# Kernel tuning notes

Hardware: AMD Instinct MI355X
Metric: run time of the kernel (lower is better)

## Reference

```python
import math
import jax, jax.numpy as jnp
import numpy as np

B, T, D, HS = 8, 2048, 1024, 64  # batch, seq (== block_size), d_embed, head_size
BLOCK_SIZE = 2048


def setup_inputs() -> dict:
    key = jax.random.key(0)
    kx, kq, kk, kv = jax.random.split(key, 4)
    x = jax.random.normal(kx, (B, T, D), dtype=jnp.float32)
    Wq = jax.random.normal(kq, (D, HS), dtype=jnp.float32) * (1.0 / math.sqrt(D))
    Wk = jax.random.normal(kk, (D, HS), dtype=jnp.float32) * (1.0 / math.sqrt(D))
    Wv = jax.random.normal(kv, (D, HS), dtype=jnp.float32) * (1.0 / math.sqrt(D))
    return {"x": x, "Wq": Wq, "Wk": Wk, "Wv": Wv}


def reference(x, Wq, Wk, Wv):
    # q, k, v: [B, T, HS]
    q = jnp.einsum("btd,dh->bth", x, Wq)
    k = jnp.einsum("btd,dh->bth", x, Wk)
    v = jnp.einsum("btd,dh->bth", x, Wv)
    # NOTE: original scales by 1/sqrt(block_size), not 1/sqrt(head_size)
    scale = 1.0 / math.sqrt(BLOCK_SIZE)
    scores = jnp.einsum("bqh,bkh->bqk", q, k) * scale  # [B, T, T]
    Tq = x.shape[1]
    causal = jnp.tril(jnp.ones((Tq, Tq), dtype=bool))
    scores = jnp.where(causal[None, :, :], scores, -jnp.inf)
    attn = jax.nn.softmax(scores, axis=-1)
    return jnp.einsum("bqk,bkh->bqh", attn, v)  # [B, T, HS]
```

## Files before the change

### kernel.cpp

```cpp
#include <hip/hip_runtime.h>

typedef unsigned short u16;
typedef unsigned int u32;
typedef float f32x4 __attribute__((ext_vector_type(4)));
typedef short s16x8 __attribute__((ext_vector_type(8)));

#define MFMA_BF16(a, b, c) __builtin_amdgcn_mfma_f32_16x16x32_bf16((a), (b), (c), 0, 0, 0)


__device__ __forceinline__ u16 f2bf(float f) {
  union { float f; u32 u; } v; v.f = f;
  u32 u = v.u;
  return (u16)((u + 0x7FFFu + ((u >> 16) & 1u)) >> 16);
}

__global__ __launch_bounds__(256) void wt_convert(const float* __restrict__ Wq,
                                                  const float* __restrict__ Wk,
                                                  const float* __restrict__ Wv,
                                                  u16* __restrict__ Wt) {
  int idx = blockIdx.x * 256 + threadIdx.x;
  if (idx >= 192 * 1024) return;
  int row = idx >> 10, d = idx & 1023;
  int m = row >> 6, h = row & 63;
  const float* W = (m == 0) ? Wq : (m == 1) ? Wk : Wv;
  Wt[idx] = f2bf(W[d * 64 + h]);
}

__global__ __launch_bounds__(512) void qkv_gemm(const float* __restrict__ x,
                                                const u16* __restrict__ Wt,
                                                u16* __restrict__ qo,
                                                u16* __restrict__ ko,
                                                u16* __restrict__ vTo) {
  __shared__ u16 Xs[2][32][88];
  __shared__ u16 Ws[2][192][88];
  const int tid = threadIdx.x;
  const int lane = tid & 63, w = tid >> 6;
  const int lc = lane & 15, hi = lane >> 4;
  const int m0 = blockIdx.x * 32;
  const int msub = w >> 2;
  const int nbase = (w & 3) * 3;

  f32x4 acc[3];
#pragma unroll
  for (int i = 0; i < 3; ++i) acc[i] = (f32x4){0.f, 0.f, 0.f, 0.f};

  const int xrow = tid >> 4, xcol = (tid & 15) * 4;
  const int wr0r = tid >> 3, wr0c = (tid & 7) * 8;
  const int wr1r = (tid + 512) >> 3, wr1c = ((tid + 512) & 7) * 8;
  const int wr2r = (tid + 1024) >> 3, wr2c = ((tid + 1024) & 7) * 8;

  float4 xr;
  uint4 wv0, wv1, wv2;
  auto issue_loads = [&](int k0) {
    xr = *(const float4*)(x + (size_t)(m0 + xrow) * 1024 + k0 + xcol);
    wv0 = *(const uint4*)&Wt[wr0r * 1024 + k0 + wr0c];
    wv1 = *(const uint4*)&Wt[wr1r * 1024 + k0 + wr1c];
    wv2 = *(const uint4*)&Wt[wr2r * 1024 + k0 + wr2c];
  };
  auto write_stage = [&](int bf) {
    u32 plo = (u32)f2bf(xr.x) | ((u32)f2bf(xr.y) << 16);
    u32 phi = (u32)f2bf(xr.z) | ((u32)f2bf(xr.w) << 16);
    *(uint2*)&Xs[bf][xrow][xcol] = make_uint2(plo, phi);
    *(uint4*)&Ws[bf][wr0r][wr0c] = wv0;
    *(uint4*)&Ws[bf][wr1r][wr1c] = wv1;
    *(uint4*)&Ws[bf][wr2r][wr2c] = wv2;
  };

  issue_loads(0);
  write_stage(0);
  __syncthreads();
  int cur = 0;

  for (int t = 0; t < 16; ++t) {
    if (t < 15) issue_loads((t + 1) * 64);
#pragma unroll
    for (int ksub = 0; ksub < 2; ++ksub) {
      s16x8 a = *(const s16x8*)&Xs[cur][msub * 16 + lc][ksub * 32 + hi * 8];
#pragma unroll
      for (int j = 0; j < 3; ++j) {
        s16x8 bfrag = *(const s16x8*)&Ws[cur][(nbase + j) * 16 + lc][ksub * 32 + hi * 8];
        acc[j] = MFMA_BF16(a, bfrag, acc[j]);
      }
    }
    if (t < 15) {
      write_stage(cur ^ 1);
      __syncthreads();
      cur ^= 1;
    }
  }

#pragma unroll
  for (int j = 0; j < 3; ++j) {
    int nt = nbase + j;
#pragma unroll
    for (int r = 0; r < 4; ++r) {
      int gr = m0 + msub * 16 + hi * 4 + r;
      u16 val = f2bf(acc[j][r]);
      int n = nt * 16 + lc;
      if (nt < 4) {
        qo[gr * 64 + n] = val;
      } else if (nt < 8) {
        ko[gr * 64 + (n - 64)] = val;
      } else {
        int b = gr >> 11, t2 = gr & 2047;
        vTo[((b << 6) + (n - 128)) * 2048 + t2] = val;
      }
    }
  }
}

__global__ __launch_bounds__(1024) void attn_fwd(const u16* __restrict__ qb,
                                                 const u16* __restrict__ kb,
                                                 const u16* __restrict__ vT,
                                                 float* __restrict__ out) {
  __shared__ u16 P[16][16][40];
  __shared__ float Po[16][16][66];
  __shared__ float Pl[16][16];
  const int tid = threadIdx.x, lane = tid & 63, w = tid >> 6;
  const int lc = lane & 15, hi = lane >> 4;
  const int q = w >> 2, s = w & 3;
  const int bid = blockIdx.x;
  const int b = bid & 7, pr = bid >> 3;
  const int tile = (q < 2) ? pr : 63 - pr;
  const int qbase = tile * 32 + (q & 1) * 16;
  const int brow = b * 2048;

  const u16* qrow = qb + (size_t)(brow + qbase + lc) * 64;
  s16x8 aq0 = *(const s16x8*)(qrow + hi * 8);
  s16x8 aq1 = *(const s16x8*)(qrow + 32 + hi * 8);

  f32x4 o[4];
  float lrow[4] = {0.f, 0.f, 0.f, 0.f};
#pragma unroll
  for (int i = 0; i < 4; ++i) o[i] = (f32x4){0.f, 0.f, 0.f, 0.f};

  const float SL = 0.031879357f;
  const int n = (qbase + 47) >> 5;
  const int c = (n + 3) >> 2;
  const int it0 = s * c;
  const int it1 = min(it0 + c, n);

  const u16* kbase = kb + (size_t)brow * 64;
  s16x8 k00, k01, k10, k11;
  if (it0 < it1) {
    const u16* krow = kbase + (size_t)(it0 * 32) * 64;
    k00 = *(const s16x8*)(krow + lc * 64 + hi * 8);
    k01 = *(const s16x8*)(krow + lc * 64 + 32 + hi * 8);
    k10 = *(const s16x8*)(krow + (16 + lc) * 64 + hi * 8);
    k11 = *(const s16x8*)(krow + (16 + lc) * 64 + 32 + hi * 8);
  }

  for (int it = it0; it < it1; ++it) {
    const int kvb = it * 32;
    s16x8 n00, n01, n10, n11;
    if (it + 1 < it1) {
      const u16* krow = kbase + (size_t)(kvb + 32) * 64;
      n00 = *(const s16x8*)(krow + lc * 64 + hi * 8);
      n01 = *(const s16x8*)(krow + lc * 64 + 32 + hi * 8);
      n10 = *(const s16x8*)(krow + (16 + lc) * 64 + hi * 8);
      n11 = *(const s16x8*)(krow + (16 + lc) * 64 + 32 + hi * 8);
    }
    f32x4 s0 = {0.f, 0.f, 0.f, 0.f}, s1 = {0.f, 0.f, 0.f, 0.f};
    s0 = MFMA_BF16(aq0, k00, s0);
    s0 = MFMA_BF16(aq1, k01, s0);
    s1 = MFMA_BF16(aq0, k10, s1);
    s1 = MFMA_BF16(aq1, k11, s1);

    s16x8 bv[4];
#pragma unroll
    for (int nt = 0; nt < 4; ++nt)
      bv[nt] = *(const s16x8*)&vT[(size_t)(b * 64 + nt * 16 + lc) * 2048 + kvb + hi * 8];

#pragma unroll
    for (int r = 0; r < 4; ++r) {
      const int qt = qbase + hi * 4 + r;
      const int kv0 = kvb + lc;
      float p0 = (kv0 <= qt) ? exp2f(s0[r] * SL) : 0.f;
      float p1 = (kv0 + 16 <= qt) ? exp2f(s1[r] * SL) : 0.f;
      lrow[r] += p0 + p1;
      P[w][hi * 4 + r][lc] = f2bf(p0);
      P[w][hi * 4 + r][16 + lc] = f2bf(p1);
    }
    asm volatile("s_waitcnt lgkmcnt(0)" ::: "memory");
    s16x8 pa = *(const s16x8*)&P[w][lc][hi * 8];
#pragma unroll
    for (int nt = 0; nt < 4; ++nt) o[nt] = MFMA_BF16(pa, bv[nt], o[nt]);

    if (it + 1 < it1) { k00 = n00; k01 = n01; k10 = n10; k11 = n11; }
  }

#pragma unroll
  for (int r = 0; r < 4; ++r) {
    lrow[r] += __shfl_xor(lrow[r], 1);
    lrow[r] += __shfl_xor(lrow[r], 2);
    lrow[r] += __shfl_xor(lrow[r], 4);
    lrow[r] += __shfl_xor(lrow[r], 8);
  }

  if (lc == 0) {
#pragma unroll
    for (int r = 0; r < 4; ++r) Pl[w][hi * 4 + r] = lrow[r];
  }
#pragma unroll
  for (int nt = 0; nt < 4; ++nt) {
#pragma unroll
    for (int r = 0; r < 4; ++r) Po[w][hi * 4 + r][nt * 16 + lc] = o[nt][r];
  }
  __syncthreads();

  if (s == 0) {
#pragma unroll 4
    for (int row = 0; row < 16; ++row) {
      float L = Pl[w][row] + Pl[w + 1][row] + Pl[w + 2][row] + Pl[w + 3][row];
      float val = Po[w][row][lane] + Po[w + 1][row][lane] +
                  Po[w + 2][row][lane] + Po[w + 3][row][lane];
      out[(size_t)(brow + qbase + row) * 64 + lane] = val / L;
    }
  }
}

extern "C" void kernel_launch(void* const* d_in, const int* in_sizes, int n_in,
                              void* d_out, int out_size, void* d_ws, size_t ws_size,
                              hipStream_t stream) {
  (void)in_sizes; (void)n_in; (void)out_size; (void)ws_size;
  const float* x = (const float*)d_in[0];
  const float* Wq = (const float*)d_in[1];
  const float* Wk = (const float*)d_in[2];
  const float* Wv = (const float*)d_in[3];
  float* out = (float*)d_out;

  u16* wsu = (u16*)d_ws;
  u16* Wt = wsu;
  u16* qb = Wt + 192 * 1024;
  u16* kb = qb + 8 * 2048 * 64;
  u16* vT = kb + 8 * 2048 * 64;

  wt_convert<<<768, 256, 0, stream>>>(Wq, Wk, Wv, Wt);
  qkv_gemm<<<512, 512, 0, stream>>>(x, Wt, qb, kb, vT);
  attn_fwd<<<256, 1024, 0, stream>>>(qb, kb, vT, out);
}
```

Measured before the change: 62.59 us.

## Rework weight transpose, load GEMM weights to registers, split attention across more waves

The weight convert kernel now transposes through shared memory in 64x64 tiles with coalesced vector reads and writes, using far fewer blocks. The QKV GEMM drops the shared-memory weight stage and loads B fragments straight from global into registers with double buffering. Attention switches to 16-row query tiles, each split across 8 key-range waves (512 blocks), adds a mask-free fast path for fully visible blocks, and uses truncating bf16 conversion for P. The combine step reuses one unioned shared buffer. Risks are more register pressure, extra cross-wave reduction work, and slightly lower P precision from truncation.

Result: slower. 132.8 us (+112.1%).

```diff
diff --git a/kernel.cpp b/kernel.cpp
--- a/kernel.cpp
+++ b/kernel.cpp
@@ -13,26 +13,51 @@
   u32 u = v.u;
   return (u16)((u + 0x7FFFu + ((u >> 16) & 1u)) >> 16);
 }
+__device__ __forceinline__ u16 f2bf_t(float f) {
+  union { float f; u32 u; } v; v.f = f;
+  return (u16)(v.u >> 16);
+}
 
 __global__ __launch_bounds__(256) void wt_convert(const float* __restrict__ Wq,
                                                   const float* __restrict__ Wk,
                                                   const float* __restrict__ Wv,
                                                   u16* __restrict__ Wt) {
-  int idx = blockIdx.x * 256 + threadIdx.x;
-  if (idx >= 192 * 1024) return;
-  int row = idx >> 10, d = idx & 1023;
-  int m = row >> 6, h = row & 63;
+  __shared__ u16 Ls[64][70];
+  const int bid = blockIdx.x;
+  const int m = bid >> 4, d0 = (bid & 15) * 64;
   const float* W = (m == 0) ? Wq : (m == 1) ? Wk : Wv;
-  Wt[idx] = f2bf(W[d * 64 + h]);
-}
-
-__global__ __launch_bounds__(512) void qkv_gemm(const float* __restrict__ x,
-                                                const u16* __restrict__ Wt,
-                                                u16* __restrict__ qo,
-                                                u16* __restrict__ ko,
-                                                u16* __restrict__ vTo) {
-  __shared__ u16 Xs[2][32][88];
-  __shared__ u16 Ws[2][192][88];
+  const int t = threadIdx.x;
+  {
+    const int dr = t >> 2, hc = (t & 3) * 16;
+    const float4* src = (const float4*)(W + (size_t)(d0 + dr) * 64 + hc);
+    float4 f0 = src[0], f1 = src[1], f2 = src[2], f3 = src[3];
+    float fl[16] = {f0.x, f0.y, f0.z, f0.w, f1.x, f1.y, f1.z, f1.w,
+                    f2.x, f2.y, f2.z, f2.w, f3.x, f3.y, f3.z, f3.w};
+#pragma unroll
+    for (int j = 0; j < 8; ++j) {
+      u32 pk = (u32)f2bf(fl[2 * j]) | ((u32)f2bf(fl[2 * j + 1]) << 16);
+      *(u32*)&Ls[dr][hc + 2 * j] = pk;
+    }
+  }
+  __syncthreads();
+  {
+    const int h = t >> 2, dcs = (t & 3) * 16;
+    u32 po[8];
+#pragma unroll
+    for (int j = 0; j < 8; ++j)
+      po[j] = (u32)Ls[dcs + 2 * j][h] | ((u32)Ls[dcs + 2 * j + 1][h] << 16);
+    uint4* dst = (uint4*)&Wt[(size_t)(m * 64 + h) * 1024 + d0 + dcs];
+    dst[0] = make_uint4(po[0], po[1], po[2], po[3]);
+    dst[1] = make_uint4(po[4], po[5], po[6], po[7]);
+  }
+}
+
+__global__ __launch_bounds__(512, 4) void qkv_gemm(const float* __restrict__ x,
+                                                   const u16* __restrict__ Wt,
+                                                   u16* __restrict__ qo,
+                                                   u16* __restrict__ ko,
+                                                   u16* __restrict__ vTo) {
+  __shared__ u16 Xs[2][32][72];
   const int tid = threadIdx.x;
   const int lane = tid & 63, w = tid >> 6;
   const int lc = lane & 15, hi = lane >> 4;
@@ -45,45 +70,45 @@
   for (int i = 0; i < 3; ++i) acc[i] = (f32x4){0.f, 0.f, 0.f, 0.f};
 
   const int xrow = tid >> 4, xcol = (tid & 15) * 4;
-  const int wr0r = tid >> 3, wr0c = (tid & 7) * 8;
-  const int wr1r = (tid + 512) >> 3, wr1c = ((tid + 512) & 7) * 8;
-  const int wr2r = (tid + 1024) >> 3, wr2c = ((tid + 1024) & 7) * 8;
+  size_t bofs[6];
+#pragma unroll
+  for (int j = 0; j < 3; ++j)
+#pragma unroll
+    for (int ks = 0; ks < 2; ++ks)
+      bofs[j * 2 + ks] = (size_t)((nbase + j) * 16 + lc) * 1024 + ks * 32 + hi * 8;
 
   float4 xr;
-  uint4 wv0, wv1, wv2;
-  auto issue_loads = [&](int k0) {
-    xr = *(const float4*)(x + (size_t)(m0 + xrow) * 1024 + k0 + xcol);
-    wv0 = *(const uint4*)&Wt[wr0r * 1024 + k0 + wr0c];
-    wv1 = *(const uint4*)&Wt[wr1r * 1024 + k0 + wr1c];
-    wv2 = *(const uint4*)&Wt[wr2r * 1024 + k0 + wr2c];
-  };
-  auto write_stage = [&](int bf) {
+  s16x8 bc[6], bn[6];
+  xr = *(const float4*)(x + (size_t)(m0 + xrow) * 1024 + xcol);
+#pragma unroll
+  for (int i = 0; i < 6; ++i) bc[i] = *(const s16x8*)(Wt + bofs[i]);
+  {
     u32 plo = (u32)f2bf(xr.x) | ((u32)f2bf(xr.y) << 16);
     u32 phi = (u32)f2bf(xr.z) | ((u32)f2bf(xr.w) << 16);
-    *(uint2*)&Xs[bf][xrow][xcol] = make_uint2(plo, phi);
-    *(uint4*)&Ws[bf][wr0r][wr0c] = wv0;
-    *(uint4*)&Ws[bf][wr1r][wr1c] = wv1;
-    *(uint4*)&Ws[bf][wr2r][wr2c] = wv2;
-  };
-
-  issue_loads(0);
-  write_stage(0);
+    *(uint2*)&Xs[0][xrow][xcol] = make_uint2(plo, phi);
+  }
   __syncthreads();
   int cur = 0;
 
   for (int t = 0; t < 16; ++t) {
-    if (t < 15) issue_loads((t + 1) * 64);
+    if (t < 15) {
+      const int k1 = (t + 1) * 64;
+      xr = *(const float4*)(x + (size_t)(m0 + xrow) * 1024 + k1 + xcol);
+#pragma unroll
+      for (int i = 0; i < 6; ++i) bn[i] = *(const s16x8*)(Wt + bofs[i] + k1);
+    }
 #pragma unroll
     for (int ksub = 0; ksub < 2; ++ksub) {
       s16x8 a = *(const s16x8*)&Xs[cur][msub * 16 + lc][ksub * 32 + hi * 8];
 #pragma unroll
-      for (int j = 0; j < 3; ++j) {
-        s16x8 bfrag = *(const s16x8*)&Ws[cur][(nbase + j) * 16 + lc][ksub * 32 + hi * 8];
-        acc[j] = MFMA_BF16(a, bfrag, acc[j]);
-      }
+      for (int j = 0; j < 3; ++j) acc[j] = MFMA_BF16(a, bc[j * 2 + ksub], acc[j]);
     }
     if (t < 15) {
-      write_stage(cur ^ 1);
+      u32 plo = (u32)f2bf(xr.x) | ((u32)f2bf(xr.y) << 16);
+      u32 phi = (u32)f2bf(xr.z) | ((u32)f2bf(xr.w) << 16);
+      *(uint2*)&Xs[cur ^ 1][xrow][xcol] = make_uint2(plo, phi);
+#pragma unroll
+      for (int i = 0; i < 6; ++i) bc[i] = bn[i];
       __syncthreads();
       cur ^= 1;
     }
@@ -109,21 +134,20 @@
   }
 }
 
-__global__ __launch_bounds__(1024) void attn_fwd(const u16* __restrict__ qb,
-                                                 const u16* __restrict__ kb,
-                                                 const u16* __restrict__ vT,
-                                                 float* __restrict__ out) {
-  __shared__ u16 P[16][16][40];
-  __shared__ float Po[16][16][66];
+__global__ __launch_bounds__(1024, 8) void attn_fwd(const u16* __restrict__ qb,
+                                                    const u16* __restrict__ kb,
+                                                    const u16* __restrict__ vT,
+                                                    float* __restrict__ out) {
+  __shared__ u32 U[16][1056];
   __shared__ float Pl[16][16];
   const int tid = threadIdx.x, lane = tid & 63, w = tid >> 6;
   const int lc = lane & 15, hi = lane >> 4;
-  const int q = w >> 2, s = w & 3;
+  const int q = w >> 3, s = w & 7;
   const int bid = blockIdx.x;
-  const int b = bid & 7, pr = bid >> 3;
-  const int tile = (q < 2) ? pr : 63 - pr;
-  const int qbase = tile * 32 + (q & 1) * 16;
+  const int b = bid & 7, u = bid >> 3;
+  const int qbase = (q ? (127 - u) : u) * 16;
   const int brow = b * 2048;
+  u16* Pw = (u16*)&U[w][0];
 
   const u16* qrow = qb + (size_t)(brow + qbase + lc) * 64;
   s16x8 aq0 = *(const s16x8*)(qrow + hi * 8);
@@ -136,7 +160,7 @@
 
   const float SL = 0.031879357f;
   const int n = (qbase + 47) >> 5;
-  const int c = (n + 3) >> 2;
+  const int c = (n + 7) >> 3;
   const int it0 = s * c;
   const int it1 = min(it0 + c, n);
 
@@ -171,18 +195,29 @@
     for (int nt = 0; nt < 4; ++nt)
       bv[nt] = *(const s16x8*)&vT[(size_t)(b * 64 + nt * 16 + lc) * 2048 + kvb + hi * 8];
 
-#pragma unroll
-    for (int r = 0; r < 4; ++r) {
-      const int qt = qbase + hi * 4 + r;
-      const int kv0 = kvb + lc;
-      float p0 = (kv0 <= qt) ? exp2f(s0[r] * SL) : 0.f;
-      float p1 = (kv0 + 16 <= qt) ? exp2f(s1[r] * SL) : 0.f;
-      lrow[r] += p0 + p1;
-      P[w][hi * 4 + r][lc] = f2bf(p0);
-      P[w][hi * 4 + r][16 + lc] = f2bf(p1);
+    if (kvb + 31 <= qbase) {
+#pragma unroll
+      for (int r = 0; r < 4; ++r) {
+        float p0 = exp2f(s0[r] * SL);
+        float p1 = exp2f(s1[r] * SL);
+        lrow[r] += p0 + p1;
+        Pw[(hi * 4 + r) * 40 + lc] = f2bf_t(p0);
+        Pw[(hi * 4 + r) * 40 + 16 + lc] = f2bf_t(p1);
+      }
+    } else {
+#pragma unroll
+      for (int r = 0; r < 4; ++r) {
+        const int qt = qbase + hi * 4 + r;
+        const int kv0 = kvb + lc;
+        float p0 = (kv0 <= qt) ? exp2f(s0[r] * SL) : 0.f;
+        float p1 = (kv0 + 16 <= qt) ? exp2f(s1[r] * SL) : 0.f;
+        lrow[r] += p0 + p1;
+        Pw[(hi * 4 + r) * 40 + lc] = f2bf_t(p0);
+        Pw[(hi * 4 + r) * 40 + 16 + lc] = f2bf_t(p1);
+      }
     }
     asm volatile("s_waitcnt lgkmcnt(0)" ::: "memory");
-    s16x8 pa = *(const s16x8*)&P[w][lc][hi * 8];
+    s16x8 pa = *(const s16x8*)&Pw[lc * 40 + hi * 8];
 #pragma unroll
     for (int nt = 0; nt < 4; ++nt) o[nt] = MFMA_BF16(pa, bv[nt], o[nt]);
 
@@ -201,19 +236,24 @@
 #pragma unroll
     for (int r = 0; r < 4; ++r) Pl[w][hi * 4 + r] = lrow[r];
   }
+  float* Pow = (float*)&U[w][0];
 #pragma unroll
   for (int nt = 0; nt < 4; ++nt) {
 #pragma unroll
-    for (int r = 0; r < 4; ++r) Po[w][hi * 4 + r][nt * 16 + lc] = o[nt][r];
+    for (int r = 0; r < 4; ++r) Pow[(hi * 4 + r) * 66 + nt * 16 + lc] = o[nt][r];
   }
   __syncthreads();
 
-  if (s == 0) {
-#pragma unroll 4
-    for (int row = 0; row < 16; ++row) {
-      float L = Pl[w][row] + Pl[w + 1][row] + Pl[w + 2][row] + Pl[w + 3][row];
-      float val = Po[w][row][lane] + Po[w + 1][row][lane] +
-                  Po[w + 2][row][lane] + Po[w + 3][row][lane];
+  if (s < 4) {
+#pragma unroll
+    for (int rr = 0; rr < 4; ++rr) {
+      const int row = s * 4 + rr;
+      float L = 0.f, val = 0.f;
+#pragma unroll
+      for (int j = 0; j < 8; ++j) {
+        L += Pl[q * 8 + j][row];
+        val += ((const float*)&U[q * 8 + j][0])[row * 66 + lane];
+      }
       out[(size_t)(brow + qbase + row) * 64 + lane] = val / L;
     }
   }
@@ -235,7 +275,7 @@
   u16* kb = qb + 8 * 2048 * 64;
   u16* vT = kb + 8 * 2048 * 64;
 
-  wt_convert<<<768, 256, 0, stream>>>(Wq, Wk, Wv, Wt);
+  wt_convert<<<48, 256, 0, stream>>>(Wq, Wk, Wv, Wt);
   qkv_gemm<<<512, 512, 0, stream>>>(x, Wt, qb, kb, vT);
-  attn_fwd<<<256, 1024, 0, stream>>>(qb, kb, vT, out);
-}
+  attn_fwd<<<512, 1024, 0, stream>>>(qb, kb, vT, out);
+}
```
